# Optimization experiments

Measured on AMD Instinct MI355X. Metric: run time of the kernel, lower is better.

## Reference

```python
import jax, jax.numpy as jnp
import numpy as np

N, D, C, T = 8192, 64, 100, 30  # samples, embedding_dim, n_classes, n_transforms (initialize_radial_flow n_transforms=30)
LOG_EV_CLAMP = 10.0             # EvidenceScaler clamp on log evidence
EV_BUDGET = 0.5 * D * float(np.log(4.0 * np.pi))  # 'normal' evidence budget: 0.5*dim*log(4*pi)


def setup_inputs() -> dict:
    key = jax.random.key(0)
    ks = jax.random.split(key, 8)
    x = jax.random.normal(ks[0], (N, D), dtype=jnp.float32)          # embeddings (base = identity here)
    labels = jax.random.randint(ks[1], (N,), 0, C)                   # int class labels
    freq = jax.random.uniform(ks[2], (C,), dtype=jnp.float32) + 0.1
    freq = freq / freq.sum()                                         # labels_frequency (sums to 1)
    # per-class radial flow params: z0 [C,T,D], alpha' [C,T], beta' [C,T]
    z0 = jax.random.normal(ks[3], (C, T, D), dtype=jnp.float32) * 0.1
    alpha_prime = jax.random.normal(ks[4], (C, T), dtype=jnp.float32) * 0.1
    beta_prime = jax.random.normal(ks[5], (C, T), dtype=jnp.float32) * 0.1
    W = jax.random.normal(ks[6], (D, C), dtype=jnp.float32) / np.sqrt(D)  # CategoricalOutput linear
    b = jnp.zeros((C,), jnp.float32)
    return dict(x=x, labels=labels, labels_frequency=freq, z0=z0,
                alpha_prime=alpha_prime, beta_prime=beta_prime, W=W, b=b)


def _flow_log_prob(x, z0s, aps, bps):
    """Radial normalizing flow log-density (density direction): log N(f(x)) + log|det df/dx|.
    x: [N, D]; z0s: [T, D]; aps, bps: [T]."""
    def step(carry, params):
        z, ld = carry
        z0, ap, bp = params
        alpha = jax.nn.softplus(ap)
        beta = -alpha + jax.nn.softplus(bp)   # beta > -alpha ensures invertibility
        diff = z - z0                          # [N, D]
        r = jnp.linalg.norm(diff, axis=-1)     # [N]
        h = 1.0 / (alpha + r)
        bh = beta * h
        z_new = z + bh[:, None] * diff
        # log|det| = (D-1)*log(1+beta*h) + log(1 + beta*h + beta*h'*r), h' = -h^2
        ld_new = ld + (D - 1) * jnp.log1p(bh) + jnp.log1p(bh * (1.0 - h * r))
        return (z_new, ld_new), None

    init = (x, jnp.zeros(x.shape[0], x.dtype))
    (z, ld), _ = jax.lax.scan(step, init, (z0s, aps, bps))
    base = -0.5 * (D * jnp.log(2.0 * jnp.pi) + jnp.sum(z * z, axis=-1))  # standard normal base
    return base + ld


def reference(x, labels, labels_frequency, z0, alpha_prime, beta_prime, W, b):
    # per-class flow log-probs for ALL samples: [C, N] (dispatch-compute, vectorized over classes)
    lp = jax.vmap(_flow_log_prob, in_axes=(None, 0, 0, 0))(x, z0, alpha_prime, beta_prime)
    # class_specific_log_prob: gather each sample's own-class log-prob (the boolean-mask gather/scatter loop)
    class_lp = jnp.take_along_axis(lp, labels[None, :], axis=0)[0]            # [N]
    # marginalize_log_prob: logsumexp over classes with log class frequencies
    marg = jax.nn.logsumexp(lp + jnp.log(labels_frequency)[:, None], axis=0)  # [N]
    # EvidenceScaler('normal') + clamp, then NatPN Dirichlet posterior update
    log_ev = jnp.minimum(marg + EV_BUDGET, LOG_EV_CLAMP)                      # [N]
    probs = jax.nn.softmax(x @ W + b, axis=-1)                                # expected sufficient statistics
    alpha = 1.0 + jnp.exp(log_ev)[:, None] * probs                            # prior alpha=1 + evidence*stats
    # output: [N, C+1] = [log alpha | class-specific log-prob]
    return jnp.concatenate([jnp.log(alpha), class_lp[:, None]], axis=1)
```

## Files before the change

kernel.cpp:

```cpp
#include <hip/hip_runtime.h>
#include <math.h>

#define N 8192
#define D 64
#define C 100
#define T 30
#define GSTRIDE 32
#define ZROWS 32
#define CROWS 112
#define WSTRIDE 20
#define SB 16

static constexpr float D_LOG_2PI      = 117.62413225019811f;
static constexpr float EV_BUDGET_F    = 80.992775903017304f;
static constexpr float LOG_EV_CLAMP_F = 10.0f;

typedef __attribute__((ext_vector_type(8))) short short8x;
typedef __attribute__((ext_vector_type(4))) float floatx4;

static __device__ __forceinline__ unsigned short f2bf(float f) {
    __bf16 h = (__bf16)f;
    return __builtin_bit_cast(unsigned short, h);
}

__global__ __launch_bounds__(256) void megaprep_kernel(
        const float* __restrict__ x,
        const float* __restrict__ z0,
        const float* __restrict__ ap,
        const float* __restrict__ bp,
        const float* __restrict__ W,
        unsigned short* __restrict__ xbf,
        float* __restrict__ q0,
        float* __restrict__ Gp,
        float* __restrict__ alphas,
        float* __restrict__ betas,
        unsigned short* __restrict__ z0bf,
        unsigned short* __restrict__ wtbf) {
    const int blk = blockIdx.x;

    if (blk < 256) {
        const int r = blk * 32 + (threadIdx.x >> 3);
        const int e = threadIdx.x & 7;
        const float4* xp = (const float4*)(x + (size_t)r * D + e * 8);
        const float4 a = xp[0], b = xp[1];
        short8x o;
        o[0] = f2bf(a.x); o[1] = f2bf(a.y); o[2] = f2bf(a.z); o[3] = f2bf(a.w);
        o[4] = f2bf(b.x); o[5] = f2bf(b.y); o[6] = f2bf(b.z); o[7] = f2bf(b.w);
        *(short8x*)(xbf + (size_t)r * D + e * 8) = o;
        float q = a.x*a.x + a.y*a.y + a.z*a.z + a.w*a.w
                + b.x*b.x + b.y*b.y + b.z*b.z + b.w*b.w;
        q += __shfl_xor(q, 4, 8);
        q += __shfl_xor(q, 2, 8);
        q += __shfl_xor(q, 1, 8);
        if (e == 0) q0[r] = q;
        return;
    }

    if (blk >= 356) {
        const int i = (blk - 356) * 256 + threadIdx.x;
        const int c = i >> 6, d = i & 63;
        wtbf[i] = f2bf(c < C ? W[d * C + c] : 0.0f);
        return;
    }

    const int c = blk - 256;
    __shared__ float z0s[T * D];
    for (int i = threadIdx.x; i < T * D; i += blockDim.x)
        z0s[i] = z0[c * T * D + i];
    __syncthreads();

    for (int idx = threadIdx.x; idx < T * T; idx += blockDim.x) {
        const int u = idx / T, v = idx % T;
        float s = 0.0f;
        #pragma unroll
        for (int d = 0; d < D; ++d)
            s = fmaf(z0s[u * D + d], z0s[v * D + d], s);
        Gp[(size_t)c * T * GSTRIDE + u * GSTRIDE + v] = s;
    }

    for (int i = threadIdx.x; i < ZROWS * D; i += blockDim.x) {
        const int u = i >> 6;
        z0bf[(size_t)c * ZROWS * D + i] = f2bf(u < T ? z0s[u * D + (i & 63)] : 0.0f);
    }

    if (threadIdx.x < T) {
        const float a = ap[c * T + threadIdx.x];
        const float b = bp[c * T + threadIdx.x];
        const float spa = fmaxf(a, 0.0f) + log1pf(expf(-fabsf(a)));
        const float spb = fmaxf(b, 0.0f) + log1pf(expf(-fabsf(b)));
        alphas[c * T + threadIdx.x] = spa;
        betas[c * T + threadIdx.x]  = -spa + spb;
    }
}

__global__ __launch_bounds__(256, 2) void flow_kernel(
        const unsigned short* __restrict__ xbf,
        const float* __restrict__ q0g,
        const unsigned short* __restrict__ z0bf,
        const float* __restrict__ Gp,
        const float* __restrict__ alphas,
        const float* __restrict__ betas,
        float* __restrict__ lp) {
    const int c    = blockIdx.y;
    const int wv   = threadIdx.x >> 6;
    const int ln   = threadIdx.x & 63;
    const int col  = ln & 15;
    const int quad = ln >> 4;
    const int nb   = blockIdx.x * 256 + wv * 64;
    const int n    = nb + ln;

    __shared__ float Gs[T * GSTRIDE];
    __shared__ float ab[64];
    __shared__ float wlds[4][64 * WSTRIDE];

    for (int i = threadIdx.x; i < T * GSTRIDE; i += 256)
        Gs[i] = Gp[(size_t)c * T * GSTRIDE + i];
    if (threadIdx.x < T) ab[threadIdx.x] = alphas[c * T + threadIdx.x];
    else if (threadIdx.x >= 32 && threadIdx.x < 32 + T)
        ab[threadIdx.x] = betas[c * T + (threadIdx.x - 32)];
    __syncthreads();

    const unsigned short* zb = z0bf + (size_t)c * ZROWS * D;
    float w[ZROWS];

    #pragma unroll
    for (int mu = 0; mu < 2; ++mu) {
        const short8x A0 = *(const short8x*)(zb + (mu * 16 + col) * D + quad * 8);
        const short8x A1 = *(const short8x*)(zb + (mu * 16 + col) * D + 32 + quad * 8);
        floatx4 acc[4];
        #pragma unroll
        for (int nt = 0; nt < 4; ++nt) acc[nt] = (floatx4)(0.0f);
        #pragma unroll
        for (int nt = 0; nt < 4; ++nt) {
            const unsigned short* bp_ = xbf + (size_t)(nb + nt * 16 + col) * D + quad * 8;
            const short8x B0 = *(const short8x*)(bp_);
            acc[nt] = __builtin_amdgcn_mfma_f32_16x16x32_bf16(A0, B0, acc[nt], 0, 0, 0);
            const short8x B1 = *(const short8x*)(bp_ + 32);
            acc[nt] = __builtin_amdgcn_mfma_f32_16x16x32_bf16(A1, B1, acc[nt], 0, 0, 0);
        }
        #pragma unroll
        for (int nt = 0; nt < 4; ++nt)
            *(floatx4*)&wlds[wv][(nt * 16 + col) * WSTRIDE + quad * 4] = acc[nt];
        #pragma unroll
        for (int j = 0; j < 4; ++j) {
            const float4 t = *(const float4*)&wlds[wv][ln * WSTRIDE + j * 4];
            w[mu * 16 + 4 * j + 0] = t.x; w[mu * 16 + 4 * j + 1] = t.y;
            w[mu * 16 + 4 * j + 2] = t.z; w[mu * 16 + 4 * j + 3] = t.w;
        }
    }

    float q    = q0g[n];
    float P    = 1.0f;
    float prod = 1.0f;
    float ld   = 0.0f;
    #pragma unroll
    for (int t = 0; t < T; ++t) {
        const float Gtt   = Gs[t * GSTRIDE + t];
        const float alpha = ab[t];
        const float beta  = ab[32 + t];
        const float wt    = P * w[t];
        float r2 = fmaf(-2.0f, wt, q) + Gtt;
        r2 = fmaxf(r2, 0.0f);
        const float r  = __builtin_amdgcn_sqrtf(r2);
        const float h  = __builtin_amdgcn_rcpf(alpha + r);
        const float bh = beta * h;
        const float f  = 1.0f + bh;
        const float f2 = f * f, f4 = f2 * f2, f8 = f4 * f4;
        const float f16 = f8 * f8, f32v = f16 * f16;
        float p = f32v * f16; p *= f8; p *= f4; p *= f2; p *= f;
        p *= fmaf(bh * alpha, h, 1.0f);
        prod *= p;
        if ((t % 6) == 5) { ld += __logf(prod); prod = 1.0f; }
        const float m = bh * f;
        float qn = f2 * q;
        qn = fmaf(m, -2.0f * wt, qn);
        qn = fmaf(bh * bh, Gtt, qn);
        q = qn;
        const float Pn = P * f;
        const float k  = bh * __builtin_amdgcn_rcpf(Pn);
        #pragma unroll
        for (int m4 = 0; m4 < 8; ++m4) {
            if (m4 < (t >> 2)) continue;
            const float4 g = *(const float4*)&Gs[t * GSTRIDE + 4 * m4];
            w[4 * m4 + 0] = fmaf(-k, g.x, w[4 * m4 + 0]);
            w[4 * m4 + 1] = fmaf(-k, g.y, w[4 * m4 + 1]);
            w[4 * m4 + 2] = fmaf(-k, g.z, w[4 * m4 + 2]);
            w[4 * m4 + 3] = fmaf(-k, g.w, w[4 * m4 + 3]);
        }
        P = Pn;
    }
    ld += __logf(prod);

    lp[(size_t)c * N + n] = -0.5f * (D_LOG_2PI + q) + ld;
}

__global__ __launch_bounds__(256) void epilogue_kernel(
        const float* __restrict__ lp,
        const unsigned short* __restrict__ xbf,
        const unsigned short* __restrict__ wtbf,
        const float* __restrict__ b,
        const int* __restrict__ labels,
        const float* __restrict__ freq,
        float* __restrict__ out) {
    const int n0  = blockIdx.x * SB;
    const int tid = threadIdx.x;
    const int wv  = tid >> 6;
    const int ln  = tid & 63;

    __shared__ float lps[SB][101];
    __shared__ float lgs[SB][CROWS];
    __shared__ float lf[C];
    __shared__ float bsm[C];
    __shared__ int   lbl[SB];

    if (wv == 0) {
        const int col  = ln & 15;
        const int quad = ln >> 4;
        const unsigned short* bp_ = xbf + (size_t)(n0 + col) * D + quad * 8;
        const short8x B0 = *(const short8x*)(bp_);
        const short8x B1 = *(const short8x*)(bp_ + 32);
        #pragma unroll
        for (int ct = 0; ct < 7; ++ct) {
            const unsigned short* apq = wtbf + (size_t)(ct * 16 + col) * D + quad * 8;
            const short8x A0 = *(const short8x*)(apq);
            const short8x A1 = *(const short8x*)(apq + 32);
            floatx4 acc = (floatx4)(0.0f);
            acc = __builtin_amdgcn_mfma_f32_16x16x32_bf16(A0, B0, acc, 0, 0, 0);
            acc = __builtin_amdgcn_mfma_f32_16x16x32_bf16(A1, B1, acc, 0, 0, 0);
            #pragma unroll
            for (int j = 0; j < 4; ++j)
                lgs[col][ct * 16 + quad * 4 + j] = acc[j];
        }
    } else {
        for (int i = tid - 64; i < C * SB; i += 192) {
            const int cc = i >> 4, s = i & (SB - 1);
            lps[s][cc] = lp[(size_t)cc * N + n0 + s];
        }
        if (tid - 64 < C) {
            const int t2 = tid - 64;
            lf[t2]  = __logf(freq[t2]);
            bsm[t2] = b[t2];
        }
        if (tid >= 192 && tid < 192 + SB)
            lbl[tid - 192] = labels[n0 + (tid - 192)];
    }
    __syncthreads();

    const int s = tid >> 4;
    const int k = tid & 15;
    const int n = n0 + s;

    float lgt[7];
    float lm = -INFINITY;
    float vm = -INFINITY, vs = 0.0f;
    #pragma unroll
    for (int j = 0; j < 7; ++j) {
        const int cc = k + 16 * j;
        if (cc < C) {
            const float v = lps[s][cc] + lf[cc];
            const float m2 = fmaxf(vm, v);
            vs = vs * __expf(vm - m2) + __expf(v - m2);
            vm = m2;
            lgt[j] = lgs[s][cc] + bsm[cc];
            lm = fmaxf(lm, lgt[j]);
        } else lgt[j] = -INFINITY;
    }

    #pragma unroll
    for (int off = 8; off >= 1; off >>= 1) {
        const float om = __shfl_xor(vm, off, 16);
        const float os = __shfl_xor(vs, off, 16);
        const float m2 = fmaxf(vm, om);
        vs = vs * __expf(vm - m2) + os * __expf(om - m2);
        vm = m2;
        lm = fmaxf(lm, __shfl_xor(lm, off, 16));
    }
    const float marg = vm + __logf(vs);
    const float ev = __expf(fminf(marg + EV_BUDGET_F, LOG_EV_CLAMP_F));

    float ls = 0.0f;
    #pragma unroll
    for (int j = 0; j < 7; ++j)
        if (k + 16 * j < C) ls += __expf(lgt[j] - lm);
    #pragma unroll
    for (int off = 8; off >= 1; off >>= 1)
        ls += __shfl_xor(ls, off, 16);

    const float inv = ev / ls;
    float* __restrict__ outr = out + (size_t)n * (C + 1);
    #pragma unroll
    for (int j = 0; j < 7; ++j) {
        const int cc = k + 16 * j;
        if (cc < C) outr[cc] = log1pf(__expf(lgt[j] - lm) * inv);
    }
    if (k == 0) outr[C] = lps[s][lbl[s]];
}

extern "C" void kernel_launch(void* const* d_in, const int* in_sizes, int n_in,
                              void* d_out, int out_size, void* d_ws, size_t ws_size,
                              hipStream_t stream) {
    const float* x      = (const float*)d_in[0];
    const int*   labels = (const int*)  d_in[1];
    const float* freq   = (const float*)d_in[2];
    const float* z0     = (const float*)d_in[3];
    const float* ap     = (const float*)d_in[4];
    const float* bp     = (const float*)d_in[5];
    const float* W      = (const float*)d_in[6];
    const float* b      = (const float*)d_in[7];
    float* out = (float*)d_out;

    float* ws     = (float*)d_ws;
    float* lp     = ws;
    float* Gp     = lp + (size_t)C * N;
    float* alphas = Gp + (size_t)C * T * GSTRIDE;
    float* betas  = alphas + (size_t)C * T;
    unsigned short* z0bf = (unsigned short*)(betas + (size_t)C * T);
    unsigned short* xbf  = z0bf + (size_t)C * ZROWS * D;
    unsigned short* wtbf = xbf + (size_t)N * D;
    float* q0     = (float*)(wtbf + (size_t)CROWS * D);

    megaprep_kernel<<<384, 256, 0, stream>>>(x, z0, ap, bp, W,
                                             xbf, q0, Gp, alphas, betas, z0bf, wtbf);
    flow_kernel<<<dim3(N / 256, C), 256, 0, stream>>>(xbf, q0, z0bf, Gp, alphas, betas, lp);
    epilogue_kernel<<<N / SB, 256, 0, stream>>>(lp, xbf, wtbf, b, labels, freq, out);
}
```

Baseline: 151.5 us.

## Process two samples per thread in flow kernel and simplify log-det accumulation

Each thread now advances two samples through the 30 radial-flow steps. Every Gs row load from LDS and every per-step alpha/beta/Gtt fetch is shared by both samples, and the two dependency chains can interleave. The per-step f^63 power chain is replaced by running products of f and of the second factor, with a single 63*log at the end. The per-step scalars are packed into one float4 in shared memory, and the grid is halved. The cost is doubled register pressure for the w arrays, fewer blocks to fill the GPU, and some risk that the long running products lose precision.

```diff
diff --git a/kernel.cpp b/kernel.cpp
--- a/kernel.cpp
+++ b/kernel.cpp
@@ -106,92 +106,125 @@
     const int ln   = threadIdx.x & 63;
     const int col  = ln & 15;
     const int quad = ln >> 4;
-    const int nb   = blockIdx.x * 256 + wv * 64;
-    const int n    = nb + ln;
+    const int nb   = blockIdx.x * 512 + wv * 128;
 
     __shared__ float Gs[T * GSTRIDE];
-    __shared__ float ab[64];
+    __shared__ float abg[T * 4];
     __shared__ float wlds[4][64 * WSTRIDE];
 
     for (int i = threadIdx.x; i < T * GSTRIDE; i += 256)
         Gs[i] = Gp[(size_t)c * T * GSTRIDE + i];
-    if (threadIdx.x < T) ab[threadIdx.x] = alphas[c * T + threadIdx.x];
-    else if (threadIdx.x >= 32 && threadIdx.x < 32 + T)
-        ab[threadIdx.x] = betas[c * T + (threadIdx.x - 32)];
+    if (threadIdx.x < T) {
+        const int t = threadIdx.x;
+        abg[t * 4 + 0] = alphas[c * T + t];
+        abg[t * 4 + 1] = betas[c * T + t];
+        abg[t * 4 + 2] = Gp[(size_t)c * T * GSTRIDE + t * GSTRIDE + t];
+        abg[t * 4 + 3] = 0.0f;
+    }
     __syncthreads();
 
     const unsigned short* zb = z0bf + (size_t)c * ZROWS * D;
-    float w[ZROWS];
-
+    short8x A[2][2];
     #pragma unroll
     for (int mu = 0; mu < 2; ++mu) {
-        const short8x A0 = *(const short8x*)(zb + (mu * 16 + col) * D + quad * 8);
-        const short8x A1 = *(const short8x*)(zb + (mu * 16 + col) * D + 32 + quad * 8);
-        floatx4 acc[4];
+        A[mu][0] = *(const short8x*)(zb + (mu * 16 + col) * D + quad * 8);
+        A[mu][1] = *(const short8x*)(zb + (mu * 16 + col) * D + 32 + quad * 8);
+    }
+
+    float w[2][ZROWS];
+    #pragma unroll
+    for (int half = 0; half < 2; ++half) {
+        const int hb = nb + half * 64;
         #pragma unroll
-        for (int nt = 0; nt < 4; ++nt) acc[nt] = (floatx4)(0.0f);
-        #pragma unroll
-        for (int nt = 0; nt < 4; ++nt) {
-            const unsigned short* bp_ = xbf + (size_t)(nb + nt * 16 + col) * D + quad * 8;
-            const short8x B0 = *(const short8x*)(bp_);
-            acc[nt] = __builtin_amdgcn_mfma_f32_16x16x32_bf16(A0, B0, acc[nt], 0, 0, 0);
-            const short8x B1 = *(const short8x*)(bp_ + 32);
-            acc[nt] = __builtin_amdgcn_mfma_f32_16x16x32_bf16(A1, B1, acc[nt], 0, 0, 0);
-        }
-        #pragma unroll
-        for (int nt = 0; nt < 4; ++nt)
-            *(floatx4*)&wlds[wv][(nt * 16 + col) * WSTRIDE + quad * 4] = acc[nt];
-        #pragma unroll
-        for (int j = 0; j < 4; ++j) {
-            const float4 t = *(const float4*)&wlds[wv][ln * WSTRIDE + j * 4];
-            w[mu * 16 + 4 * j + 0] = t.x; w[mu * 16 + 4 * j + 1] = t.y;
-            w[mu * 16 + 4 * j + 2] = t.z; w[mu * 16 + 4 * j + 3] = t.w;
-        }
-    }
-
-    float q    = q0g[n];
-    float P    = 1.0f;
-    float prod = 1.0f;
-    float ld   = 0.0f;
+        for (int mu = 0; mu < 2; ++mu) {
+            floatx4 acc[4];
+            #pragma unroll
+            for (int nt = 0; nt < 4; ++nt) acc[nt] = (floatx4)(0.0f);
+            #pragma unroll
+            for (int nt = 0; nt < 4; ++nt) {
+                const unsigned short* bp_ =
+                    xbf + (size_t)(hb + nt * 16 + col) * D + quad * 8;
+                const short8x B0 = *(const short8x*)(bp_);
+                acc[nt] = __builtin_amdgcn_mfma_f32_16x16x32_bf16(A[mu][0], B0, acc[nt], 0, 0, 0);
+                const short8x B1 = *(const short8x*)(bp_ + 32);
+                acc[nt] = __builtin_amdgcn_mfma_f32_16x16x32_bf16(A[mu][1], B1, acc[nt], 0, 0, 0);
+            }
+            #pragma unroll
+            for (int nt = 0; nt < 4; ++nt)
+                *(floatx4*)&wlds[wv][(nt * 16 + col) * WSTRIDE + quad * 4] = acc[nt];
+            #pragma unroll
+            for (int j = 0; j < 4; ++j) {
+                const float4 t = *(const float4*)&wlds[wv][ln * WSTRIDE + j * 4];
+                w[half][mu * 16 + 4 * j + 0] = t.x;
+                w[half][mu * 16 + 4 * j + 1] = t.y;
+                w[half][mu * 16 + 4 * j + 2] = t.z;
+                w[half][mu * 16 + 4 * j + 3] = t.w;
+            }
+        }
+    }
+
+    float qA = q0g[nb + ln], qB = q0g[nb + 64 + ln];
+    float PA = 1.0f, PB = 1.0f;
+    float pfA = 1.0f, pfB = 1.0f;
+    float pgA = 1.0f, pgB = 1.0f;
     #pragma unroll
     for (int t = 0; t < T; ++t) {
-        const float Gtt   = Gs[t * GSTRIDE + t];
-        const float alpha = ab[t];
-        const float beta  = ab[32 + t];
-        const float wt    = P * w[t];
-        float r2 = fmaf(-2.0f, wt, q) + Gtt;
-        r2 = fmaxf(r2, 0.0f);
-        const float r  = __builtin_amdgcn_sqrtf(r2);
-        const float h  = __builtin_amdgcn_rcpf(alpha + r);
-        const float bh = beta * h;
-        const float f  = 1.0f + bh;
-        const float f2 = f * f, f4 = f2 * f2, f8 = f4 * f4;
-        const float f16 = f8 * f8, f32v = f16 * f16;
-        float p = f32v * f16; p *= f8; p *= f4; p *= f2; p *= f;
-        p *= fmaf(bh * alpha, h, 1.0f);
-        prod *= p;
-        if ((t % 6) == 5) { ld += __logf(prod); prod = 1.0f; }
-        const float m = bh * f;
-        float qn = f2 * q;
-        qn = fmaf(m, -2.0f * wt, qn);
-        qn = fmaf(bh * bh, Gtt, qn);
-        q = qn;
-        const float Pn = P * f;
-        const float k  = bh * __builtin_amdgcn_rcpf(Pn);
+        const floatx4 av = *(const floatx4*)&abg[t * 4];
+        const float alpha = av[0], beta = av[1], Gtt = av[2];
+
+        const float wtA = PA * w[0][t];
+        float r2A = fmaf(-2.0f, wtA, qA) + Gtt;
+        r2A = fmaxf(r2A, 0.0f);
+        const float rA  = __builtin_amdgcn_sqrtf(r2A);
+        const float hA  = __builtin_amdgcn_rcpf(alpha + rA);
+        const float bhA = beta * hA;
+        const float fA  = 1.0f + bhA;
+        pfA *= fA;
+        pgA *= fmaf(bhA * alpha, hA, 1.0f);
+        float qnA = fA * fA * qA;
+        qnA = fmaf(bhA * fA, -2.0f * wtA, qnA);
+        qnA = fmaf(bhA * bhA, Gtt, qnA);
+        qA = qnA;
+        const float PnA = PA * fA;
+        const float kA  = bhA * __builtin_amdgcn_rcpf(PnA);
+        PA = PnA;
+
+        const float wtB = PB * w[1][t];
+        float r2B = fmaf(-2.0f, wtB, qB) + Gtt;
+        r2B = fmaxf(r2B, 0.0f);
+        const float rB  = __builtin_amdgcn_sqrtf(r2B);
+        const float hB  = __builtin_amdgcn_rcpf(alpha + rB);
+        const float bhB = beta * hB;
+        const float fB  = 1.0f + bhB;
+        pfB *= fB;
+        pgB *= fmaf(bhB * alpha, hB, 1.0f);
+        float qnB = fB * fB * qB;
+        qnB = fmaf(bhB * fB, -2.0f * wtB, qnB);
+        qnB = fmaf(bhB * bhB, Gtt, qnB);
+        qB = qnB;
+        const float PnB = PB * fB;
+        const float kB  = bhB * __builtin_amdgcn_rcpf(PnB);
+        PB = PnB;
+
         #pragma unroll
         for (int m4 = 0; m4 < 8; ++m4) {
             if (m4 < (t >> 2)) continue;
             const float4 g = *(const float4*)&Gs[t * GSTRIDE + 4 * m4];
-            w[4 * m4 + 0] = fmaf(-k, g.x, w[4 * m4 + 0]);
-            w[4 * m4 + 1] = fmaf(-k, g.y, w[4 * m4 + 1]);
-            w[4 * m4 + 2] = fmaf(-k, g.z, w[4 * m4 + 2]);
-            w[4 * m4 + 3] = fmaf(-k, g.w, w[4 * m4 + 3]);
-        }
-        P = Pn;
-    }
-    ld += __logf(prod);
-
-    lp[(size_t)c * N + n] = -0.5f * (D_LOG_2PI + q) + ld;
+            w[0][4 * m4 + 0] = fmaf(-kA, g.x, w[0][4 * m4 + 0]);
+            w[0][4 * m4 + 1] = fmaf(-kA, g.y, w[0][4 * m4 + 1]);
+            w[0][4 * m4 + 2] = fmaf(-kA, g.z, w[0][4 * m4 + 2]);
+            w[0][4 * m4 + 3] = fmaf(-kA, g.w, w[0][4 * m4 + 3]);
+            w[1][4 * m4 + 0] = fmaf(-kB, g.x, w[1][4 * m4 + 0]);
+            w[1][4 * m4 + 1] = fmaf(-kB, g.y, w[1][4 * m4 + 1]);
+            w[1][4 * m4 + 2] = fmaf(-kB, g.z, w[1][4 * m4 + 2]);
+            w[1][4 * m4 + 3] = fmaf(-kB, g.w, w[1][4 * m4 + 3]);
+        }
+    }
+    const float ldA = 63.0f * __logf(pfA) + __logf(pgA);
+    const float ldB = 63.0f * __logf(pfB) + __logf(pgB);
+
+    lp[(size_t)c * N + nb + ln]      = -0.5f * (D_LOG_2PI + qA) + ldA;
+    lp[(size_t)c * N + nb + 64 + ln] = -0.5f * (D_LOG_2PI + qB) + ldB;
 }
 
 __global__ __launch_bounds__(256) void epilogue_kernel(
@@ -321,6 +354,6 @@
 
     megaprep_kernel<<<384, 256, 0, stream>>>(x, z0, ap, bp, W,
                                              xbf, q0, Gp, alphas, betas, z0bf, wtbf);
-    flow_kernel<<<dim3(N / 256, C), 256, 0, stream>>>(xbf, q0, z0bf, Gp, alphas, betas, lp);
+    flow_kernel<<<dim3(N / 512, C), 256, 0, stream>>>(xbf, q0, z0bf, Gp, alphas, betas, lp);
     epilogue_kernel<<<N / SB, 256, 0, stream>>>(lp, xbf, wtbf, b, labels, freq, out);
 }
```

New measurement: 128.6 us (median of 4 runs). 15.1% less time.
